# Optimization experiments

Hardware: AMD Instinct MI355X
Metric: run time of the kernel (lower is better)

The kernel has to match this reference:

```python
import jax, jax.numpy as jnp
import numpy as np

T, B, IN, H, OUT = 128, 128, 512, 512, 512


def _lstm_dir(x, W_ih, W_hh, b_ih, b_hh):
    # x: [T, B, IN]; W_ih: [4H, IN]; W_hh: [4H, H]; biases: [4H]
    # Precompute input contribution for all timesteps in one big GEMM.
    xw = jnp.einsum('tbi,gi->tbg', x, W_ih) + b_ih + b_hh  # [T, B, 4H]
    Hh = W_hh.shape[1]

    def step(carry, xw_t):
        h, c = carry
        gates = xw_t + h @ W_hh.T  # [B, 4H]
        i, f, g, o = jnp.split(gates, 4, axis=-1)  # PyTorch gate order i,f,g,o
        i = jax.nn.sigmoid(i)
        f = jax.nn.sigmoid(f)
        g = jnp.tanh(g)
        o = jax.nn.sigmoid(o)
        c = f * c + i * g
        h = o * jnp.tanh(c)
        return (h, c), h

    h0 = jnp.zeros((x.shape[1], Hh), x.dtype)
    c0 = jnp.zeros((x.shape[1], Hh), x.dtype)
    _, hs = jax.lax.scan(step, (h0, c0), xw)
    return hs  # [T, B, H]


def setup_inputs() -> dict:
    key = jax.random.key(0)
    ks = jax.random.split(key, 12)
    s_in = 1.0 / np.sqrt(H)
    u = lambda k, shape: jax.random.uniform(k, shape, jnp.float32, -s_in, s_in)
    return {
        'x': jax.random.normal(ks[0], (T, B, IN), jnp.float32),
        'W_ih_f': u(ks[1], (4 * H, IN)),
        'W_hh_f': u(ks[2], (4 * H, H)),
        'b_ih_f': u(ks[3], (4 * H,)),
        'b_hh_f': u(ks[4], (4 * H,)),
        'W_ih_b': u(ks[5], (4 * H, IN)),
        'W_hh_b': u(ks[6], (4 * H, H)),
        'b_ih_b': u(ks[7], (4 * H,)),
        'b_hh_b': u(ks[8], (4 * H,)),
        'W_lin': u(ks[9], (OUT, 2 * H)),
        'b_lin': u(ks[10], (OUT,)),
    }


def reference(x, W_ih_f, W_hh_f, b_ih_f, b_hh_f, W_ih_b, W_hh_b, b_ih_b, b_hh_b, W_lin, b_lin):
    h_fwd = _lstm_dir(x, W_ih_f, W_hh_f, b_ih_f, b_hh_f)                    # [T,B,H]
    h_bwd = _lstm_dir(x[::-1], W_ih_b, W_hh_b, b_ih_b, b_hh_b)[::-1]        # [T,B,H]
    out = jnp.concatenate([h_fwd, h_bwd], axis=-1)                          # [T,B,2H]
    out = jnp.einsum('tbh,oh->tbo', out, W_lin) + b_lin                     # [T,B,OUT]
    return out
```

## Files before the change

### kernel.cpp

```cpp
#include <hip/hip_runtime.h>

typedef unsigned short u16;
typedef unsigned long long u64;
typedef __attribute__((ext_vector_type(8))) short bf16x8;
typedef __attribute__((ext_vector_type(4))) float f32x4;

#define MFMA16(a, b, c) __builtin_amdgcn_mfma_f32_16x16x32_bf16((a), (b), (c), 0, 0, 0)

#define TT 128
#define BB 128
#define IN_ 512
#define HH 512
#define G4 2048
#define OUTD 512
#define TB 16384

#define AEXLD(p) __hip_atomic_load((p), __ATOMIC_RELAXED, __HIP_MEMORY_SCOPE_AGENT)

__device__ __forceinline__ u16 f2bf(float f) {
    union { float f; unsigned u; } v; v.f = f;
    unsigned r = v.u + 0x7FFFu + ((v.u >> 16) & 1u);
    return (u16)(r >> 16);
}
__device__ __forceinline__ float bf2f(u16 h) {
    union { unsigned u; float f; } v; v.u = ((unsigned)h) << 16; return v.f;
}
__device__ __forceinline__ float sigmoid_f(float x) { return 1.f / (1.f + __expf(-x)); }
__device__ __forceinline__ float tanh_f(float x) {
    float e = __expf(2.f * x);
    return 1.f - 2.f / (e + 1.f);
}

typedef unsigned __attribute__((address_space(1))) guint;
typedef unsigned __attribute__((address_space(3))) luint;
__device__ __forceinline__ void gll16(const u16* g, u16* l) {
    __builtin_amdgcn_global_load_lds((guint*)(void*)g, (luint*)(void*)l, 16, 0, 0);
}

__global__ void prep_kernel(
    const float* __restrict__ x,
    const float* __restrict__ Wihf, const float* __restrict__ Wihb,
    const float* __restrict__ Whhf, const float* __restrict__ Whhb,
    const float* __restrict__ Wlin,
    const float* __restrict__ bihf, const float* __restrict__ bhhf,
    const float* __restrict__ bihb, const float* __restrict__ bhhb,
    u16* __restrict__ x_bf, u16* __restrict__ wih_cat,
    u16* __restrict__ whhf_bf, u16* __restrict__ whhb_bf,
    u16* __restrict__ wlin_bf, float* __restrict__ bias_cat,
    uint4* __restrict__ exch) {
    const int i0 = blockIdx.x * blockDim.x + threadIdx.x;
    const int stride = gridDim.x * blockDim.x;
    #define CVT4(SRC, DST, N4, DOFF)                                        \
        for (int i = i0; i < (N4); i += stride) {                           \
            float4 v = ((const float4*)(SRC))[i];                           \
            ushort4 o;                                                      \
            o.x = f2bf(v.x); o.y = f2bf(v.y);                               \
            o.z = f2bf(v.z); o.w = f2bf(v.w);                               \
            ((ushort4*)(DST))[(DOFF) + i] = o;                              \
        }
    CVT4(x, x_bf, (TB * IN_) / 4, 0)
    CVT4(Wihf, wih_cat, (G4 * IN_) / 4, 0)
    CVT4(Wihb, wih_cat, (G4 * IN_) / 4, (G4 * IN_) / 4)
    CVT4(Whhf, whhf_bf, (G4 * HH) / 4, 0)
    CVT4(Whhb, whhb_bf, (G4 * HH) / 4, 0)
    CVT4(Wlin, wlin_bf, (OUTD * 2 * HH) / 4, 0)
    #undef CVT4
    for (int i = i0; i < G4; i += stride) {
        bias_cat[i]      = bihf[i] + bhhf[i];
        bias_cat[G4 + i] = bihb[i] + bhhb[i];
    }
    for (int i = i0; i < 65536; i += stride)
        exch[i] = uint4{0u, 0u, 0u, 0u};
}

__global__ __launch_bounds__(256) void gemm_bias_kernel(
    const u16* __restrict__ A, const u16* __restrict__ W,
    const float* __restrict__ bias, void* __restrict__ Cout,
    int M, int N, int K, int out_is_bf16) {
    __shared__ __align__(16) u16 lA[128 * 64];
    __shared__ __align__(16) u16 lB[128 * 64];
    const int tid = threadIdx.x;
    const int m0 = blockIdx.x * 128;
    const int n0 = blockIdx.y * 128;
    const int wave = tid >> 6, lane = tid & 63;
    const int wm = wave >> 1, wn = wave & 1;
    const int lrow = lane & 15, lq = lane >> 4;
    const int srow = lane >> 3;
    const int ssw  = (lane & 7) ^ srow;

    f32x4 acc[4][4] = {};

    for (int kc = 0; kc < K; kc += 64) {
        #pragma unroll
        for (int i = 0; i < 4; ++i) {
            int chunk = wave + i * 4;
            int row = chunk * 8 + srow;
            gll16(&A[(size_t)(m0 + row) * K + kc + ssw * 8], &lA[chunk * 512]);
            gll16(&W[(size_t)(n0 + row) * K + kc + ssw * 8], &lB[chunk * 512]);
        }
        __syncthreads();
        #pragma unroll
        for (int ks = 0; ks < 2; ++ks) {
            bf16x8 af[4], bfr[4];
            #pragma unroll
            for (int mf = 0; mf < 4; ++mf) {
                int row = wm * 64 + mf * 16 + lrow;
                int c16 = (ks * 4 + lq) ^ (row & 7);
                af[mf] = *(const bf16x8*)(&lA[row * 64 + c16 * 8]);
            }
            #pragma unroll
            for (int nf = 0; nf < 4; ++nf) {
                int row = wn * 64 + nf * 16 + lrow;
                int c16 = (ks * 4 + lq) ^ (row & 7);
                bfr[nf] = *(const bf16x8*)(&lB[row * 64 + c16 * 8]);
            }
            #pragma unroll
            for (int mf = 0; mf < 4; ++mf)
                #pragma unroll
                for (int nf = 0; nf < 4; ++nf)
                    acc[mf][nf] = MFMA16(af[mf], bfr[nf], acc[mf][nf]);
        }
        __syncthreads();
    }

    #pragma unroll
    for (int mf = 0; mf < 4; ++mf) {
        #pragma unroll
        for (int nf = 0; nf < 4; ++nf) {
            int row = m0 + wm * 64 + mf * 16 + lq * 4;
            int col = n0 + wn * 64 + nf * 16 + lrow;
            float bv = bias[col];
            f32x4 v = acc[mf][nf];
            #pragma unroll
            for (int r = 0; r < 4; ++r) {
                float val = v[r] + bv;
                if (out_is_bf16)
                    ((u16*)Cout)[(size_t)(row + r) * N + col] = f2bf(val);
                else
                    ((float*)Cout)[(size_t)(row + r) * N + col] = val;
            }
        }
    }
}

__global__ __launch_bounds__(256, 1) void lstm_persist_kernel(
    const u16* __restrict__ xw, const u16* __restrict__ whh_f,
    const u16* __restrict__ whh_b, u16* __restrict__ hcat,
    u64* __restrict__ exch) {
    const int bx = blockIdx.x;
    const int dir = bx >> 7;
    const int bt = (bx >> 4) & 7;
    const int jt = bx & 15;
    const u16* __restrict__ whh = dir ? whh_b : whh_f;
    const int b0 = bt * 16;
    const int j0 = jt * 32;

    __shared__ __align__(16) u16 lh[16 * 520];
    __shared__ float sgate[4][16][33];

    const int tid = threadIdx.x;
    const int wave = tid >> 6, lane = tid & 63;
    const int lrow = lane & 15, lq = lane >> 4;

    const u16* wrow = whh + ((size_t)wave * HH + j0) * HH;
    bf16x8 w0[16], w1[16];
    #pragma unroll
    for (int kc = 0; kc < 16; ++kc) {
        w0[kc] = *(const bf16x8*)(&wrow[(size_t)lrow * HH + kc * 32 + lq * 8]);
        w1[kc] = *(const bf16x8*)(&wrow[(size_t)(16 + lrow) * HH + kc * 32 + lq * 8]);
    }
    #pragma unroll
    for (int kc = 0; kc < 16; ++kc)
        asm volatile("" : "+v"(w0[kc]), "+v"(w1[kc]));

    const int bl = tid >> 4;
    const int jj = (tid & 15) * 2;
    float cr0 = 0.f, cr1 = 0.f;

    const size_t my_ex = ((size_t)dir * BB + b0 + bl) * 256 + (j0 >> 1) + (tid & 15);

    for (int s = 0; s < TT; ++s) {
        const int t = dir ? (TT - 1 - s) : s;

        const u16* xrow = xw + ((size_t)t * BB + b0 + bl) * (2 * G4) + dir * G4 + j0 + jj;
        unsigned xg[4];
        #pragma unroll
        for (int g = 0; g < 4; ++g)
            xg[g] = *(const unsigned*)(xrow + (size_t)g * HH);

        f32x4 acc0 = {}, acc1 = {}, acc0b = {}, acc1b = {};
        if (s > 0) {
            const int p = (s - 1) & 1;
            const u64* ex = exch + ((size_t)(p * 2 + dir) * BB + b0) * 256 + tid;
            const u64 expect = ((u64)(unsigned)s << 48) | ((u64)(unsigned)s << 16);
            u64 v[16];
            for (;;) {
                #pragma unroll
                for (int i = 0; i < 16; ++i)
                    v[i] = AEXLD(ex + (size_t)i * 256);
                bool ok = true;
                #pragma unroll
                for (int i = 0; i < 16; ++i)
                    ok &= ((v[i] & 0xFFFF0000FFFF0000ull) == expect);
                if (ok) break;
            }
            #pragma unroll
            for (int i = 0; i < 16; ++i)
                *(unsigned*)(&lh[i * 520 + tid * 2]) =
                    (unsigned)(v[i] & 0xffffu) | (unsigned)((v[i] >> 16) & 0xffff0000u);
            __syncthreads();

            #pragma unroll
            for (int kc = 0; kc < 16; kc += 2) {
                bf16x8 a0 = *(const bf16x8*)(&lh[lrow * 520 + kc * 32 + lq * 8]);
                bf16x8 a1 = *(const bf16x8*)(&lh[lrow * 520 + (kc + 1) * 32 + lq * 8]);
                acc0  = MFMA16(a0, w0[kc], acc0);
                acc1  = MFMA16(a0, w1[kc], acc1);
                acc0b = MFMA16(a1, w0[kc + 1], acc0b);
                acc1b = MFMA16(a1, w1[kc + 1], acc1b);
            }
            acc0 += acc0b;
            acc1 += acc1b;
        }

        #pragma unroll
        for (int r = 0; r < 4; ++r) {
            sgate[wave][lq * 4 + r][lrow]      = acc0[r];
            sgate[wave][lq * 4 + r][16 + lrow] = acc1[r];
        }
        __syncthreads();

        float gi0 = sgate[0][bl][jj]     + bf2f((u16)(xg[0] & 0xffffu));
        float gf0 = sgate[1][bl][jj]     + bf2f((u16)(xg[1] & 0xffffu));
        float gg0 = sgate[2][bl][jj]     + bf2f((u16)(xg[2] & 0xffffu));
        float go0 = sgate[3][bl][jj]     + bf2f((u16)(xg[3] & 0xffffu));
        float gi1 = sgate[0][bl][jj + 1] + bf2f((u16)(xg[0] >> 16));
        float gf1 = sgate[1][bl][jj + 1] + bf2f((u16)(xg[1] >> 16));
        float gg1 = sgate[2][bl][jj + 1] + bf2f((u16)(xg[2] >> 16));
        float go1 = sgate[3][bl][jj + 1] + bf2f((u16)(xg[3] >> 16));

        float c0 = sigmoid_f(gf0) * cr0 + sigmoid_f(gi0) * tanh_f(gg0);
        float c1 = sigmoid_f(gf1) * cr1 + sigmoid_f(gi1) * tanh_f(gg1);
        cr0 = c0; cr1 = c1;
        float h0 = sigmoid_f(go0) * tanh_f(c0);
        float h1 = sigmoid_f(go1) * tanh_f(c1);

        unsigned hb0 = (unsigned)f2bf(h0), hb1 = (unsigned)f2bf(h1);
        unsigned tagv = (unsigned)(s + 1) << 16;
        u64 pv = (u64)(tagv | hb0) | ((u64)(tagv | hb1) << 32);
        __hip_atomic_store(exch + (size_t)((s & 1) * 2) * BB * 256 + my_ex, pv,
                           __ATOMIC_RELAXED, __HIP_MEMORY_SCOPE_AGENT);

        *(unsigned*)(hcat + ((size_t)t * BB + b0 + bl) * (2 * HH) + dir * HH + j0 + jj) =
            hb0 | (hb1 << 16);
    }
}

#define OFF_XBF    ((size_t)0)
#define OFF_WIH    (OFF_XBF  + (size_t)TB * IN_ * 2)
#define OFF_WHHF   (OFF_WIH  + (size_t)2 * G4 * IN_ * 2)
#define OFF_WHHB   (OFF_WHHF + (size_t)G4 * HH * 2)
#define OFF_WLIN   (OFF_WHHB + (size_t)G4 * HH * 2)
#define OFF_BIAS   (OFF_WLIN + (size_t)OUTD * 2 * HH * 2)
#define OFF_XW     (OFF_BIAS + (size_t)2 * G4 * 4)
#define OFF_HCAT   (OFF_XW   + (size_t)TB * 2 * G4 * 2)
#define OFF_EXCH   (OFF_HCAT + (size_t)TB * 2 * HH * 2)
#define WS_NEED    (OFF_EXCH + (size_t)2 * 2 * BB * HH * 4)

extern "C" void kernel_launch(void* const* d_in, const int* in_sizes, int n_in,
                              void* d_out, int out_size, void* d_ws, size_t ws_size,
                              hipStream_t stream) {
    (void)in_sizes; (void)n_in; (void)out_size;
    if (ws_size < WS_NEED) return;

    const float* x    = (const float*)d_in[0];
    const float* Wihf = (const float*)d_in[1];
    const float* Whhf = (const float*)d_in[2];
    const float* bihf = (const float*)d_in[3];
    const float* bhhf = (const float*)d_in[4];
    const float* Wihb = (const float*)d_in[5];
    const float* Whhb = (const float*)d_in[6];
    const float* bihb = (const float*)d_in[7];
    const float* bhhb = (const float*)d_in[8];
    const float* Wlin = (const float*)d_in[9];
    const float* blin = (const float*)d_in[10];
    float* out = (float*)d_out;

    char* ws = (char*)d_ws;
    u16* x_bf     = (u16*)(ws + OFF_XBF);
    u16* wih_cat  = (u16*)(ws + OFF_WIH);
    u16* whhf_bf  = (u16*)(ws + OFF_WHHF);
    u16* whhb_bf  = (u16*)(ws + OFF_WHHB);
    u16* wlin_bf  = (u16*)(ws + OFF_WLIN);
    float* bias_cat = (float*)(ws + OFF_BIAS);
    u16* xw   = (u16*)(ws + OFF_XW);
    u16* hcat = (u16*)(ws + OFF_HCAT);
    u64* exch = (u64*)(ws + OFF_EXCH);

    prep_kernel<<<1024, 256, 0, stream>>>(x, Wihf, Wihb, Whhf, Whhb, Wlin,
                                          bihf, bhhf, bihb, bhhb,
                                          x_bf, wih_cat, whhf_bf, whhb_bf, wlin_bf,
                                          bias_cat, (uint4*)exch);

    gemm_bias_kernel<<<dim3(TB / 128, (2 * G4) / 128), 256, 0, stream>>>(
        x_bf, wih_cat, bias_cat, xw, TB, 2 * G4, IN_, 1);

    lstm_persist_kernel<<<256, 256, 0, stream>>>(xw, whhf_bf, whhb_bf, hcat, exch);

    gemm_bias_kernel<<<dim3(TB / 128, OUTD / 128), 256, 0, stream>>>(
        hcat, wlin_bf, blin, out, TB, OUTD, 2 * HH, 0);
}
```

Baseline: 621.1 us.

## Remap LSTM blocks per XCD and poll a fast L2-local exchange buffer

Remaps block indices so the 16 blocks of one (direction, batch-tile) group land on the same XCD under round-robin dispatch. Each step's h is also published to a second exchange buffer with workgroup-scope stores, which consumers poll with sc0 loads that can hit the local L2. The agent-scope buffer is kept as a fallback after several fast polls fail. The aim is lower cross-block barrier latency per timestep, at the cost of relying on undocumented dispatch-to-XCD mapping and cache coherence behaviour, and of double stores.

```diff
diff --git a/kernel.cpp b/kernel.cpp
--- a/kernel.cpp
+++ b/kernel.cpp
@@ -35,6 +35,47 @@
 typedef unsigned __attribute__((address_space(3))) luint;
 __device__ __forceinline__ void gll16(const u16* g, u16* l) {
     __builtin_amdgcn_global_load_lds((guint*)(void*)g, (luint*)(void*)l, 16, 0, 0);
+}
+
+#define TMASK 0xFFFF0000FFFF0000ull
+__device__ __forceinline__ bool tag_ok(const u64 v[16], u64 expect) {
+    bool ok = true;
+    #pragma unroll
+    for (int i = 0; i < 16; ++i)
+        ok &= ((v[i] & TMASK) == expect);
+    return ok;
+}
+__device__ __forceinline__ void slow_volley16(const u64* b, u64 v[16]) {
+    #pragma unroll
+    for (int i = 0; i < 16; ++i)
+        v[i] = AEXLD(b + (size_t)i * 256);
+}
+__device__ __forceinline__ void fast_volley16(const u64* b, u64 v[16]) {
+    asm volatile(
+        "global_load_dwordx2 %0, %16, off sc0\n\t"
+        "global_load_dwordx2 %1, %16, off offset:2048 sc0\n\t"
+        "global_load_dwordx2 %2, %17, off sc0\n\t"
+        "global_load_dwordx2 %3, %17, off offset:2048 sc0\n\t"
+        "global_load_dwordx2 %4, %18, off sc0\n\t"
+        "global_load_dwordx2 %5, %18, off offset:2048 sc0\n\t"
+        "global_load_dwordx2 %6, %19, off sc0\n\t"
+        "global_load_dwordx2 %7, %19, off offset:2048 sc0\n\t"
+        "global_load_dwordx2 %8, %20, off sc0\n\t"
+        "global_load_dwordx2 %9, %20, off offset:2048 sc0\n\t"
+        "global_load_dwordx2 %10, %21, off sc0\n\t"
+        "global_load_dwordx2 %11, %21, off offset:2048 sc0\n\t"
+        "global_load_dwordx2 %12, %22, off sc0\n\t"
+        "global_load_dwordx2 %13, %22, off offset:2048 sc0\n\t"
+        "global_load_dwordx2 %14, %23, off sc0\n\t"
+        "global_load_dwordx2 %15, %23, off offset:2048 sc0\n\t"
+        "s_waitcnt vmcnt(0)"
+        : "=&v"(v[0]), "=&v"(v[1]), "=&v"(v[2]), "=&v"(v[3]),
+          "=&v"(v[4]), "=&v"(v[5]), "=&v"(v[6]), "=&v"(v[7]),
+          "=&v"(v[8]), "=&v"(v[9]), "=&v"(v[10]), "=&v"(v[11]),
+          "=&v"(v[12]), "=&v"(v[13]), "=&v"(v[14]), "=&v"(v[15])
+        : "v"(b), "v"(b + 512), "v"(b + 1024), "v"(b + 1536),
+          "v"(b + 2048), "v"(b + 2560), "v"(b + 3072), "v"(b + 3584)
+        : "memory");
 }
 
 __global__ void prep_kernel(
@@ -69,7 +110,7 @@
         bias_cat[i]      = bihf[i] + bhhf[i];
         bias_cat[G4 + i] = bihb[i] + bhhb[i];
     }
-    for (int i = i0; i < 65536; i += stride)
+    for (int i = i0; i < 131072; i += stride)
         exch[i] = uint4{0u, 0u, 0u, 0u};
 }
 
@@ -146,11 +187,13 @@
 __global__ __launch_bounds__(256, 1) void lstm_persist_kernel(
     const u16* __restrict__ xw, const u16* __restrict__ whh_f,
     const u16* __restrict__ whh_b, u16* __restrict__ hcat,
-    u64* __restrict__ exch) {
+    u64* __restrict__ exch, u64* __restrict__ exchf) {
     const int bx = blockIdx.x;
-    const int dir = bx >> 7;
-    const int bt = (bx >> 4) & 7;
-    const int jt = bx & 15;
+    const int slot = bx & 7;
+    const int jt  = (bx >> 3) & 15;
+    const int g   = slot + 8 * (bx >> 7);
+    const int dir = g >> 3;
+    const int bt  = g & 7;
     const u16* __restrict__ whh = dir ? whh_b : whh_f;
     const int b0 = bt * 16;
     const int j0 = jt * 32;
@@ -185,25 +228,29 @@
         const u16* xrow = xw + ((size_t)t * BB + b0 + bl) * (2 * G4) + dir * G4 + j0 + jj;
         unsigned xg[4];
         #pragma unroll
-        for (int g = 0; g < 4; ++g)
-            xg[g] = *(const unsigned*)(xrow + (size_t)g * HH);
+        for (int gg = 0; gg < 4; ++gg)
+            xg[gg] = *(const unsigned*)(xrow + (size_t)gg * HH);
 
         f32x4 acc0 = {}, acc1 = {}, acc0b = {}, acc1b = {};
         if (s > 0) {
             const int p = (s - 1) & 1;
-            const u64* ex = exch + ((size_t)(p * 2 + dir) * BB + b0) * 256 + tid;
+            const size_t ebase = ((size_t)(p * 2 + dir) * BB + b0) * 256 + tid;
+            const u64* exs = exch  + ebase;
+            const u64* exf = exchf + ebase;
             const u64 expect = ((u64)(unsigned)s << 48) | ((u64)(unsigned)s << 16);
             u64 v[16];
             for (;;) {
-                #pragma unroll
-                for (int i = 0; i < 16; ++i)
-                    v[i] = AEXLD(ex + (size_t)i * 256);
-                bool ok = true;
-                #pragma unroll
-                for (int i = 0; i < 16; ++i)
-                    ok &= ((v[i] & 0xFFFF0000FFFF0000ull) == expect);
-                if (ok) break;
-            }
+                bool got = false;
+                #pragma unroll 1
+                for (int it = 0; it < 8 && !got; ++it) {
+                    fast_volley16(exf, v);
+                    got = tag_ok(v, expect);
+                }
+                if (got) break;
+                slow_volley16(exs, v);
+                if (tag_ok(v, expect)) break;
+            }
+
             #pragma unroll
             for (int i = 0; i < 16; ++i)
                 *(unsigned*)(&lh[i * 520 + tid * 2]) =
@@ -248,8 +295,11 @@
         unsigned hb0 = (unsigned)f2bf(h0), hb1 = (unsigned)f2bf(h1);
         unsigned tagv = (unsigned)(s + 1) << 16;
         u64 pv = (u64)(tagv | hb0) | ((u64)(tagv | hb1) << 32);
-        __hip_atomic_store(exch + (size_t)((s & 1) * 2) * BB * 256 + my_ex, pv,
-                           __ATOMIC_RELAXED, __HIP_MEMORY_SCOPE_AGENT);
+        const size_t pub = (size_t)((s & 1) * 2) * BB * 256 + my_ex;
+        __hip_atomic_store(exchf + pub, pv, __ATOMIC_RELAXED,
+                           __HIP_MEMORY_SCOPE_WORKGROUP);
+        __hip_atomic_store(exch + pub, pv, __ATOMIC_RELAXED,
+                           __HIP_MEMORY_SCOPE_AGENT);
 
         *(unsigned*)(hcat + ((size_t)t * BB + b0 + bl) * (2 * HH) + dir * HH + j0 + jj) =
             hb0 | (hb1 << 16);
@@ -265,7 +315,8 @@
 #define OFF_XW     (OFF_BIAS + (size_t)2 * G4 * 4)
 #define OFF_HCAT   (OFF_XW   + (size_t)TB * 2 * G4 * 2)
 #define OFF_EXCH   (OFF_HCAT + (size_t)TB * 2 * HH * 2)
-#define WS_NEED    (OFF_EXCH + (size_t)2 * 2 * BB * HH * 4)
+#define OFF_EXCHF  (OFF_EXCH + (size_t)2 * 2 * BB * HH * 4)
+#define WS_NEED    (OFF_EXCHF + (size_t)2 * 2 * BB * HH * 4)
 
 extern "C" void kernel_launch(void* const* d_in, const int* in_sizes, int n_in,
                               void* d_out, int out_size, void* d_ws, size_t ws_size,
@@ -293,9 +344,10 @@
     u16* whhb_bf  = (u16*)(ws + OFF_WHHB);
     u16* wlin_bf  = (u16*)(ws + OFF_WLIN);
     float* bias_cat = (float*)(ws + OFF_BIAS);
-    u16* xw   = (u16*)(ws + OFF_XW);
-    u16* hcat = (u16*)(ws + OFF_HCAT);
-    u64* exch = (u64*)(ws + OFF_EXCH);
+    u16* xw    = (u16*)(ws + OFF_XW);
+    u16* hcat  = (u16*)(ws + OFF_HCAT);
+    u64* exch  = (u64*)(ws + OFF_EXCH);
+    u64* exchf = (u64*)(ws + OFF_EXCHF);
 
     prep_kernel<<<1024, 256, 0, stream>>>(x, Wihf, Wihb, Whhf, Whhb, Wlin,
                                           bihf, bhhf, bihb, bhhb,
@@ -305,7 +357,8 @@
     gemm_bias_kernel<<<dim3(TB / 128, (2 * G4) / 128), 256, 0, stream>>>(
         x_bf, wih_cat, bias_cat, xw, TB, 2 * G4, IN_, 1);
 
-    lstm_persist_kernel<<<256, 256, 0, stream>>>(xw, whhf_bf, whhb_bf, hcat, exch);
+    lstm_persist_kernel<<<256, 256, 0, stream>>>(xw, whhf_bf, whhb_bf, hcat,
+                                                 exch, exchf);
 
     gemm_bias_kernel<<<dim3(TB / 128, OUTD / 128), 256, 0, stream>>>(
         hcat, wlin_bf, blin, out, TB, OUTD, 2 * HH, 0);
```

After: 826.8 us. 33.1% more time.
